# Optimization experiments

Measured on AMD Instinct MI355X. Metric: run time of the kernel, lower is better.

Reference implementation:

```python
import jax, jax.numpy as jnp
import numpy as np

N = 50000      # nodes
E = 800000     # edges
IN = 128       # raw node feature dim
EMB = 64       # gene/pathway embedding dim
H = 256        # hidden dim
R = 12         # relations
B = 8          # num_bases (hardcoded in HRAN)
HEADS = 4      # attention heads (hardcoded)
NG = 20000     # n_gene
NPATH = 2000   # n_path
IN1 = IN + EMB # conv1 input dim


def _glorot(k, shape):
    fan_in, fan_out = shape[-2], shape[-1]
    s = np.sqrt(2.0 / (fan_in + fan_out)).astype(np.float32)
    return jax.random.normal(k, shape, jnp.float32) * s


def setup_inputs() -> dict:
    key = jax.random.key(0)
    ks = jax.random.split(key, 20)
    return {
        "x": jax.random.normal(ks[0], (N, IN), jnp.float32),
        "edge_index": jax.random.randint(ks[1], (2, E), 0, N),
        "edge_type": jax.random.randint(ks[2], (E,), 0, R),
        "gene_idx": jnp.arange(NG),
        "path_idx": jnp.arange(NPATH) + NG,  # disjoint from gene_idx
        "gene_emb": jax.random.normal(ks[3], (NG, EMB), jnp.float32) * 0.02,
        "path_emb": jax.random.normal(ks[4], (NPATH, EMB), jnp.float32) * 0.02,
        "comp1": _glorot(ks[5], (R, B)),
        "basis1": _glorot(ks[6], (B, IN1, H)),
        "root1": _glorot(ks[7], (IN1, H)),
        "bias1": jnp.zeros((H,), jnp.float32),
        "att1": _glorot(ks[8], (HEADS, H // HEADS)),
        "comp2": _glorot(ks[9], (R, B)),
        "basis2": _glorot(ks[10], (B, H, H)),
        "root2": _glorot(ks[11], (H, H)),
        "bias2": jnp.zeros((H,), jnp.float32),
        "att2": _glorot(ks[12], (HEADS, H // HEADS)),
        "pred_w": _glorot(ks[13], (H, 12)),
        "pred_b": jnp.zeros((12,), jnp.float32),
    }


def _rgcn(x, src, dst, et, comp, basis, root, bias):
    # Basis-decomposed RGCN with per-relation mean aggregation (PyG default).
    flat = dst * R + et                                   # combined (node, rel) id
    cnt = jax.ops.segment_sum(jnp.ones((src.shape[0],), jnp.float32), flat,
                              num_segments=N * R)
    w = 1.0 / jnp.maximum(cnt[flat], 1.0)                 # [E] mean normalizer
    coeff = comp[et] * w[:, None]                         # [E, B]
    xs = x[src]                                           # [E, in]  gather
    # aggregate in input space, then one dense contraction with the bases
    agg = jnp.stack([jax.ops.segment_sum(coeff[:, b, None] * xs, dst,
                                         num_segments=N)
                     for b in range(B)], axis=1)          # [N, B, in]
    return jnp.einsum('nbi,bio->no', agg, basis) + x @ root + bias


def _hran_conv(x, src, dst, et, comp, basis, root, bias, att):
    h = _rgcn(x, src, dst, et, comp, basis, root, bias)
    h = h.reshape(N, HEADS, -1)                           # [N, heads, hd]
    alpha = jax.nn.softmax((h * att).sum(-1), axis=1)     # softmax over heads
    return (h * alpha[..., None]).reshape(N, -1)


def reference(x, edge_index, edge_type, gene_idx, path_idx,
              gene_emb, path_emb,
              comp1, basis1, root1, bias1, att1,
              comp2, basis2, root2, bias2, att2,
              pred_w, pred_b):
    src, dst = edge_index[0], edge_index[1]
    x0 = jnp.concatenate([x, jnp.zeros((N, EMB), x.dtype)], axis=1)
    x0 = x0.at[gene_idx, IN:].add(gene_emb)
    x0 = x0.at[path_idx, IN:].add(path_emb)
    h = _hran_conv(x0, src, dst, edge_type, comp1, basis1, root1, bias1, att1)
    h = _hran_conv(h, src, dst, edge_type, comp2, basis2, root2, bias2, att2)
    return h @ pred_w + pred_b                            # [N, 12]
```

## Files before the change

kernel.cpp:

```cpp
#include <hip/hip_runtime.h>
#include <cstddef>

#define NN     50000
#define NE     800000
#define IND    128
#define EMBD   64
#define IN1    192
#define HDIM   256
#define RR     12
#define BB     8
#define NGENE  20000
#define NPATH  2000
#define NRK    (RR * NN)
#define SCB    1024
#define NSB    ((NRK + SCB - 1) / SCB)
#define CHA    16704
#define CHB    33408
#define CH2N   (NN - CHB)

typedef __attribute__((ext_vector_type(8))) short short8;
typedef __attribute__((ext_vector_type(4))) float f32x4;
typedef unsigned short ushortT;
typedef __attribute__((address_space(3))) void lds_void;
typedef __attribute__((address_space(1))) const void glb_void;

__device__ __forceinline__ float bu2f(unsigned short u) {
  unsigned int x = ((unsigned int)u) << 16;
  return __builtin_bit_cast(float, x);
}
__device__ __forceinline__ unsigned short f2bu(float f) {
  unsigned int x = __builtin_bit_cast(unsigned int, f);
  unsigned int r = (x + 0x7fffu + ((x >> 16) & 1u)) >> 16;
  return (unsigned short)r;
}


__global__ void k_build_x0(const float* __restrict__ x, ushortT* __restrict__ x0) {
  int t = blockIdx.x * 256 + threadIdx.x;
  if (t >= NN * IN1) return;
  int n = t / IN1, i = t - n * IN1;
  float v = (i < IND) ? x[(size_t)n * IND + i] : 0.0f;
  int kt = i >> 6, ch = (i >> 3) & 7, off = i & 7;
  x0[(size_t)n * IN1 + kt * 64 + ((ch ^ (n & 7)) * 8) + off] = f2bu(v);
}

__global__ void k_add_emb(const int* __restrict__ idx, const float* __restrict__ emb,
                          ushortT* __restrict__ x0, int count) {
  int t = blockIdx.x * 256 + threadIdx.x;
  if (t >= count * EMBD) return;
  int g = t / EMBD, j = t - g * EMBD;
  int n = idx[g];
  int ch = (j >> 3) & 7, off = j & 7;
  x0[(size_t)n * IN1 + 128 + ((ch ^ (n & 7)) * 8) + off] = f2bu(emb[t]);
}

__global__ void k_count(const int* __restrict__ ei, const int* __restrict__ et,
                        int* __restrict__ cnt) {
  int e = blockIdx.x * 256 + threadIdx.x;
  if (e >= NE) return;
  atomicAdd(&cnt[ei[NE + e] * RR + et[e]], 1);
}

__global__ __launch_bounds__(256) void k_scan1(const int* __restrict__ cnt,
                                               int* __restrict__ bsum) {
  __shared__ int lds[256];
  int t = threadIdx.x;
  int base = blockIdx.x * SCB + t * 4;
  int s = 0;
#pragma unroll
  for (int j = 0; j < 4; j++) { int idx = base + j; if (idx < NRK) s += cnt[idx]; }
  lds[t] = s; __syncthreads();
  for (int d = 128; d > 0; d >>= 1) { if (t < d) lds[t] += lds[t + d]; __syncthreads(); }
  if (t == 0) bsum[blockIdx.x] = lds[0];
}

__global__ __launch_bounds__(1024) void k_scan2(const int* __restrict__ bsum,
                                                int* __restrict__ bscan) {
  __shared__ int lds[1024];
  int t = threadIdx.x;
  int v = (t < NSB) ? bsum[t] : 0;
  lds[t] = v; __syncthreads();
  for (int d = 1; d < 1024; d <<= 1) {
    int add = (t >= d) ? lds[t - d] : 0; __syncthreads();
    lds[t] += add; __syncthreads();
  }
  if (t < NSB) bscan[t] = lds[t] - v;
}

__global__ __launch_bounds__(256) void k_scan3(const int* __restrict__ cnt,
                                               const int* __restrict__ bscan,
                                               int* __restrict__ off) {
  __shared__ int lds[256];
  int t = threadIdx.x;
  int base = blockIdx.x * SCB + t * 4;
  int v[4]; int s = 0;
#pragma unroll
  for (int j = 0; j < 4; j++) { int idx = base + j; v[j] = (idx < NRK) ? cnt[idx] : 0; s += v[j]; }
  lds[t] = s; __syncthreads();
  for (int d = 1; d < 256; d <<= 1) {
    int add = (t >= d) ? lds[t - d] : 0; __syncthreads();
    lds[t] += add; __syncthreads();
  }
  int ex = lds[t] - s + bscan[blockIdx.x];
#pragma unroll
  for (int j = 0; j < 4; j++) {
    int idx = base + j;
    if (idx < NRK) { off[idx] = ex; ex += v[j]; }
  }
}

__global__ void k_fill(const int* __restrict__ ei, const int* __restrict__ et,
                       const int* __restrict__ off, int* __restrict__ fill,
                       int* __restrict__ srcs) {
  int e = blockIdx.x * 256 + threadIdx.x;
  if (e >= NE) return;
  int key = ei[NE + e] * RR + et[e];
  int pos = off[key] + atomicAdd(&fill[key], 1);
  srcs[pos] = ei[e];
}

__global__ void k_wbasis(const float* __restrict__ basis, ushortT* __restrict__ W,
                         int in_dim) {
  int t = blockIdx.x * 256 + threadIdx.x;
  int total = BB * HDIM * in_dim;
  if (t >= total) return;
  int i = t % in_dim;
  int o = (t / in_dim) & 255;
  int b = t / (in_dim * 256);
  W[t] = f2bu(basis[((size_t)b * in_dim + i) * HDIM + o]);
}

__global__ void k_troot(const float* __restrict__ root, ushortT* __restrict__ rt,
                        int in_dim) {
  int t = blockIdx.x * 256 + threadIdx.x;
  if (t >= in_dim * HDIM) return;
  int i = t % in_dim, o = t / in_dim;
  rt[t] = f2bu(root[(size_t)i * HDIM + o]);
}


__device__ __forceinline__ void dev_aggb(const int* __restrict__ srcs,
                                         const int* __restrict__ off,
                                         const int* __restrict__ cnt,
                                         const float* __restrict__ comp,
                                         const ushortT* __restrict__ xin,
                                         ushortT* __restrict__ aggB,
                                         int in_dim, int row0, int nrows,
                                         int li, int lane) {
  if (li >= nrows) return;
  int dst = row0 + li;
  bool act = lane * 4 < in_dim;
  int kt = lane >> 4, chl = (lane >> 1) & 7, offh = (lane & 1) * 4;
  int kbase = kt * 64 + offh;

  auto gaddr = [&](int s) {
    return (const ushort4*)(xin + (size_t)s * in_dim + kbase + ((chl ^ (s & 7)) * 8));
  };

  int beg[RR], n[RR];
#pragma unroll
  for (int rl = 0; rl < RR; rl++) {
    beg[rl] = off[dst * RR + rl];
    n[rl]   = cnt[dst * RR + rl];
  }

  int sa[RR], sb[RR];
#pragma unroll
  for (int rl = 0; rl < RR; rl++) {
    sa[rl] = (n[rl] > 0) ? srcs[beg[rl]] : 0;
    sb[rl] = (n[rl] > 1) ? srcs[beg[rl] + 1] : 0;
  }

  ushort4 va[RR], vb[RR];
  if (act) {
#pragma unroll
    for (int rl = 0; rl < RR; rl++) va[rl] = *gaddr(sa[rl]);
#pragma unroll
    for (int rl = 0; rl < RR; rl++) vb[rl] = *gaddr(sb[rl]);
  }

  float acc[BB][4];
#pragma unroll
  for (int b = 0; b < BB; b++)
#pragma unroll
    for (int e = 0; e < 4; e++) acc[b][e] = 0.f;

#pragma unroll
  for (int rl = 0; rl < RR; rl++) {
    int ne = n[rl];
    if (ne == 0) continue;
    float s0 = 0.f, s1 = 0.f, s2 = 0.f, s3 = 0.f;
    if (act) {
      s0 = bu2f(va[rl].x); s1 = bu2f(va[rl].y); s2 = bu2f(va[rl].z); s3 = bu2f(va[rl].w);
      if (ne > 1) {
        s0 += bu2f(vb[rl].x); s1 += bu2f(vb[rl].y);
        s2 += bu2f(vb[rl].z); s3 += bu2f(vb[rl].w);
      }
    }
    for (int p = 2; p < ne; p++) {
      int s = srcs[beg[rl] + p];
      if (act) {
        ushort4 v = *gaddr(s);
        s0 += bu2f(v.x); s1 += bu2f(v.y); s2 += bu2f(v.z); s3 += bu2f(v.w);
      }
    }
    float wn = 1.0f / (float)ne;
#pragma unroll
    for (int b = 0; b < BB; b++) {
      float cb = comp[rl * BB + b] * wn;
      acc[b][0] += cb * s0; acc[b][1] += cb * s1;
      acc[b][2] += cb * s2; acc[b][3] += cb * s3;
    }
  }

  if (act) {
    size_t base = (size_t)li * BB * in_dim;
    int swz = (chl ^ (dst & 7)) * 8;
#pragma unroll
    for (int b = 0; b < BB; b++) {
      ushort4 o;
      o.x = f2bu(acc[b][0]); o.y = f2bu(acc[b][1]);
      o.z = f2bu(acc[b][2]); o.w = f2bu(acc[b][3]);
      *(ushort4*)(aggB + base + (size_t)b * in_dim + kbase + swz) = o;
    }
  }
}

__device__ __forceinline__ void dev_gemm(ushortT* As , float (*sm)[4],
                                         int gblk, int tid,
                                         const ushortT* __restrict__ xin,
                                         const ushortT* __restrict__ aggB,
                                         const ushortT* __restrict__ W,
                                         const float* __restrict__ bias,
                                         const float* __restrict__ att,
                                         ushortT* __restrict__ hout,
                                         int in_dim, int row0, int row1) {
  const int bm = row0 + gblk * 64;
  const int wv = tid >> 6, l = tid & 63;
  const int wc = wv;
  const int lm = l & 15, lq = l >> 4;
  const int nkt = in_dim >> 6;
  const int totKt = 9 * nkt;

  f32x4 acc[4][4];
#pragma unroll
  for (int mt = 0; mt < 4; mt++)
#pragma unroll
    for (int nt = 0; nt < 4; nt++) acc[mt][nt] = (f32x4){0.f, 0.f, 0.f, 0.f};

  struct WF { short8 f[2][4]; };
  WF w0, w1;

  auto stage = [&](int buf, int seg, int kt) {
#pragma unroll
    for (int j = 0; j < 2; j++) {
      int r = wv * 16 + j * 8;
      int g = bm + r + (l >> 3); if (g >= row1) g = row1 - 1;
      const ushortT* gp;
      if (seg == 0) gp = xin + (size_t)g * in_dim + kt * 64 + (l & 7) * 8;
      else gp = aggB + ((size_t)(g - row0) * 8 + (seg - 1)) * in_dim + kt * 64 + (l & 7) * 8;
      ushortT* lp = &As[(size_t)buf * 64 * 64 + r * 64];
      __builtin_amdgcn_global_load_lds((glb_void*)gp, (lds_void*)lp, 16, 0, 0);
    }
  };

  auto loadW = [&](WF& wd, int seg, int kt) {
    const ushortT* wt = W + (size_t)(wc * 64 + lm) * in_dim +
                        (size_t)seg * 256 * in_dim + kt * 64 + lq * 8;
#pragma unroll
    for (int nt = 0; nt < 4; nt++) {
      wd.f[0][nt] = *(const short8*)(wt + (size_t)nt * 16 * in_dim);
      wd.f[1][nt] = *(const short8*)(wt + (size_t)nt * 16 * in_dim + 32);
    }
  };

  auto mfmaT = [&](int buf, const WF& wf) {
#pragma unroll
    for (int ks = 0; ks < 2; ks++) {
      short8 af[4];
#pragma unroll
      for (int mt = 0; mt < 4; mt++) {
        int ar = mt * 16 + lm;
        af[mt] = *(const short8*)(&As[(size_t)buf * 64 * 64 + ar * 64 +
                                      (((ks * 4) + lq) ^ (ar & 7)) * 8]);
      }
#pragma unroll
      for (int mt = 0; mt < 4; mt++)
#pragma unroll
        for (int nt = 0; nt < 4; nt++)
          acc[mt][nt] = __builtin_amdgcn_mfma_f32_16x16x32_bf16(af[mt], wf.f[ks][nt],
                                                                acc[mt][nt], 0, 0, 0);
    }
  };

  int segS = 0, ktS = 0;
  int segW = 0, ktW = 0;
  auto bumpC = [&](int& s, int& k) {
    if (++k == nkt) { k = 0; if (++s == 9) { s = 8; k = nkt - 1; } }
  };

  auto body = [&](int t, WF& wuse, WF& wload) {
    loadW(wload, segW, ktW); bumpC(segW, ktW);
    asm volatile("s_waitcnt vmcnt(10)" ::: "memory");
    __builtin_amdgcn_s_barrier();
    __builtin_amdgcn_sched_barrier(0);
    stage((t + 3) & 3, segS, ktS); bumpC(segS, ktS);
    mfmaT(t & 3, wuse);
  };

  stage(0, segS, ktS); bumpC(segS, ktS);
  stage(1, segS, ktS); bumpC(segS, ktS);
  stage(2, segS, ktS); bumpC(segS, ktS);
  loadW(w0, segW, ktW); bumpC(segW, ktW);

  int t = 0;
  for (; t + 1 < totKt; t += 2) {
    body(t, w0, w1);
    body(t + 1, w1, w0);
  }
  if (t < totKt) body(t, w0, w1);
  asm volatile("s_waitcnt vmcnt(0)" ::: "memory");
  __syncthreads();

  float bv[4];
#pragma unroll
  for (int nt = 0; nt < 4; nt++) bv[nt] = bias[wc * 64 + nt * 16 + lm];
#pragma unroll
  for (int mt = 0; mt < 4; mt++)
#pragma unroll
    for (int nt = 0; nt < 4; nt++)
#pragma unroll
      for (int r = 0; r < 4; r++) acc[mt][nt][r] += bv[nt];

  float av[4];
#pragma unroll
  for (int nt = 0; nt < 4; nt++) av[nt] = att[wc * 64 + nt * 16 + lm];
#pragma unroll
  for (int mt = 0; mt < 4; mt++) {
    float sr[4];
#pragma unroll
    for (int r = 0; r < 4; r++)
      sr[r] = acc[mt][0][r] * av[0] + acc[mt][1][r] * av[1] +
              acc[mt][2][r] * av[2] + acc[mt][3][r] * av[3];
#pragma unroll
    for (int o = 1; o <= 8; o <<= 1) {
#pragma unroll
      for (int r = 0; r < 4; r++) sr[r] += __shfl_xor(sr[r], o, 64);
    }
    if (lm == 0) {
#pragma unroll
      for (int r = 0; r < 4; r++) sm[mt * 16 + lq * 4 + r][wc] = sr[r];
    }
  }
  __syncthreads();
  if (tid < 64) {
    float s0 = sm[tid][0], s1 = sm[tid][1], s2 = sm[tid][2], s3 = sm[tid][3];
    float mx = fmaxf(fmaxf(s0, s1), fmaxf(s2, s3));
    float e0 = __expf(s0 - mx), e1 = __expf(s1 - mx), e2 = __expf(s2 - mx), e3 = __expf(s3 - mx);
    float inv = 1.0f / (e0 + e1 + e2 + e3);
    sm[tid][0] = e0 * inv; sm[tid][1] = e1 * inv; sm[tid][2] = e2 * inv; sm[tid][3] = e3 * inv;
  }
  __syncthreads();
#pragma unroll
  for (int mt = 0; mt < 4; mt++) {
#pragma unroll
    for (int r = 0; r < 4; r++) {
      int rl = mt * 16 + lq * 4 + r;
      int row = bm + rl;
      if (row >= row1) continue;
      float al = sm[rl][wc];
      ushortT* op = hout + (size_t)row * HDIM + wc * 64;
      int key = row & 7;
#pragma unroll
      for (int nt = 0; nt < 4; nt++) {
        int ci = nt * 16 + lm;
        op[(((ci >> 3) ^ key) * 8) + (ci & 7)] = f2bu(acc[mt][nt][r] * al);
      }
    }
  }
}


__global__ __launch_bounds__(256) void k_aggb(const int* __restrict__ srcs,
                                              const int* __restrict__ off,
                                              const int* __restrict__ cnt,
                                              const float* __restrict__ comp,
                                              const ushortT* __restrict__ xin,
                                              ushortT* __restrict__ aggB,
                                              int in_dim, int row0, int nrows) {
  int wv = threadIdx.x >> 6, lane = threadIdx.x & 63;
  dev_aggb(srcs, off, cnt, comp, xin, aggB, in_dim, row0, nrows,
           blockIdx.x * 4 + wv, lane);
}

__global__ __launch_bounds__(256, 2) void k_gemm(const ushortT* __restrict__ xin,
                                                 const ushortT* __restrict__ aggB,
                                                 const ushortT* __restrict__ W,
                                                 const float* __restrict__ bias,
                                                 const float* __restrict__ att,
                                                 ushortT* __restrict__ hout,
                                                 int in_dim, int row0, int row1) {
  __shared__ ushortT As[4][64 * 64];
  __shared__ float sm[64][4];
  dev_gemm(&As[0][0], sm, blockIdx.x, threadIdx.x,
           xin, aggB, W, bias, att, hout, in_dim, row0, row1);
}

__global__ __launch_bounds__(256, 2) void k_fused(const ushortT* __restrict__ xin,
                                                  const ushortT* __restrict__ aggR,
                                                  const ushortT* __restrict__ W,
                                                  const float* __restrict__ bias,
                                                  const float* __restrict__ att,
                                                  ushortT* __restrict__ hout,
                                                  int in_dim, int grow0, int grow1,
                                                  int gB,
                                                  const int* __restrict__ srcs,
                                                  const int* __restrict__ off,
                                                  const int* __restrict__ cnt,
                                                  const float* __restrict__ comp,
                                                  ushortT* __restrict__ aggW,
                                                  int arow0, int anrows) {
  __shared__ ushortT As[4][64 * 64];
  __shared__ float sm[64][4];
  if ((int)blockIdx.x < gB) {
    dev_gemm(&As[0][0], sm, blockIdx.x, threadIdx.x,
             xin, aggR, W, bias, att, hout, in_dim, grow0, grow1);
  } else {
    int wv = threadIdx.x >> 6, lane = threadIdx.x & 63;
    dev_aggb(srcs, off, cnt, comp, xin, aggW, in_dim, arow0, anrows,
             ((int)blockIdx.x - gB) * 4 + wv, lane);
  }
}

__global__ void k_pred(const ushortT* __restrict__ h, const float* __restrict__ w,
                       const float* __restrict__ b, float* __restrict__ out) {
  int t = blockIdx.x * 256 + threadIdx.x;
  if (t >= NN * 12) return;
  int n = t / 12, j = t - n * 12;
  float acc = b[j];
  const ushortT* hp = h + (size_t)n * HDIM;
  int key = n & 7;
#pragma unroll
  for (int kt = 0; kt < 4; kt++)
#pragma unroll
    for (int cs = 0; cs < 8; cs++) {
      int ch = cs ^ key;
      int kb = kt * 64 + ch * 8;
      const ushortT* hh = hp + kt * 64 + cs * 8;
#pragma unroll
      for (int o = 0; o < 8; o++) acc += bu2f(hh[o]) * w[(kb + o) * 12 + j];
    }
  out[t] = acc;
}

extern "C" void kernel_launch(void* const* d_in, const int* in_sizes, int n_in,
                              void* d_out, int out_size, void* d_ws, size_t ws_size,
                              hipStream_t stream) {
  const float* x         = (const float*)d_in[0];
  const int*   edge_idx  = (const int*)d_in[1];
  const int*   edge_type = (const int*)d_in[2];
  const int*   gene_idx  = (const int*)d_in[3];
  const int*   path_idx  = (const int*)d_in[4];
  const float* gene_emb  = (const float*)d_in[5];
  const float* path_emb  = (const float*)d_in[6];
  const float* comp1     = (const float*)d_in[7];
  const float* basis1    = (const float*)d_in[8];
  const float* root1     = (const float*)d_in[9];
  const float* bias1     = (const float*)d_in[10];
  const float* att1      = (const float*)d_in[11];
  const float* comp2     = (const float*)d_in[12];
  const float* basis2    = (const float*)d_in[13];
  const float* root2     = (const float*)d_in[14];
  const float* bias2     = (const float*)d_in[15];
  const float* att2      = (const float*)d_in[16];
  const float* pred_w    = (const float*)d_in[17];
  const float* pred_b    = (const float*)d_in[18];
  float* out = (float*)d_out;

  char* ws = (char*)d_ws;
  ushortT* x0b   = (ushortT*)(ws);
  ushortT* h2b   = (ushortT*)(ws);
  ushortT* h1b   = (ushortT*)(ws + 25600000);
  ushortT* aggB0 = (ushortT*)(ws + 51200000);
  ushortT* aggB1 = (ushortT*)(ws + 119619584);
  ushortT* Wb1   = (ushortT*)(ws + 188039168);
  ushortT* Wb2   = (ushortT*)(ws + 188923904);
  int*     cnt   = (int*)(ws + 190103552);
  int*     off   = (int*)(ws + 192503552);
  int*     srcs  = (int*)(ws + 194903552);
  int*     fill  = (int*)(ws + 198103552);
  int*     bsum  = (int*)(ws + 200503552);
  int*     bscan = (int*)(ws + 200507648);

  dim3 blk(256);

  k_build_x0<<<dim3((NN * IN1) / 256), blk, 0, stream>>>(x, x0b);
  k_add_emb<<<dim3((NGENE * EMBD) / 256), blk, 0, stream>>>(gene_idx, gene_emb, x0b, NGENE);
  k_add_emb<<<dim3((NPATH * EMBD) / 256), blk, 0, stream>>>(path_idx, path_emb, x0b, NPATH);
  hipMemsetAsync(cnt, 0, NRK * 4, stream);
  hipMemsetAsync(fill, 0, NRK * 4, stream);
  k_count<<<dim3(NE / 256), blk, 0, stream>>>(edge_idx, edge_type, cnt);
  k_scan1<<<dim3(NSB), blk, 0, stream>>>(cnt, bsum);
  k_scan2<<<dim3(1), dim3(1024), 0, stream>>>(bsum, bscan);
  k_scan3<<<dim3(NSB), blk, 0, stream>>>(cnt, bscan, off);
  k_fill<<<dim3(NE / 256), blk, 0, stream>>>(edge_idx, edge_type, off, fill, srcs);
  k_troot<<<dim3((IN1 * HDIM) / 256), blk, 0, stream>>>(root1, Wb1, IN1);
  k_troot<<<dim3((HDIM * HDIM) / 256), blk, 0, stream>>>(root2, Wb2, HDIM);
  k_wbasis<<<dim3((BB * HDIM * IN1) / 256), blk, 0, stream>>>(basis1, Wb1 + 256 * IN1, IN1);
  k_wbasis<<<dim3((BB * HDIM * HDIM) / 256), blk, 0, stream>>>(basis2, Wb2 + 256 * HDIM, HDIM);

  const int gB01 = CHA / 64;
  const int gB2  = (CH2N + 63) / 64;
  const int aB01 = CHA / 4;
  const int aB2  = (CH2N + 3) / 4;

  k_aggb<<<dim3(aB01), blk, 0, stream>>>(srcs, off, cnt, comp1, x0b, aggB0, IN1, 0, CHA);
  k_fused<<<dim3(gB01 + aB01), blk, 0, stream>>>(x0b, aggB0, Wb1, bias1, att1, h1b,
                                                 IN1, 0, CHA, gB01,
                                                 srcs, off, cnt, comp1, aggB1, CHA, CHA);
  k_fused<<<dim3(gB01 + aB2), blk, 0, stream>>>(x0b, aggB1, Wb1, bias1, att1, h1b,
                                                IN1, CHA, CHB, gB01,
                                                srcs, off, cnt, comp1, aggB0, CHB, CH2N);
  k_gemm<<<dim3(gB2), blk, 0, stream>>>(x0b, aggB0, Wb1, bias1, att1, h1b, IN1, CHB, NN);

  k_aggb<<<dim3(aB01), blk, 0, stream>>>(srcs, off, cnt, comp2, h1b, aggB0, HDIM, 0, CHA);
  k_fused<<<dim3(gB01 + aB01), blk, 0, stream>>>(h1b, aggB0, Wb2, bias2, att2, h2b,
                                                 HDIM, 0, CHA, gB01,
                                                 srcs, off, cnt, comp2, aggB1, CHA, CHA);
  k_fused<<<dim3(gB01 + aB2), blk, 0, stream>>>(h1b, aggB1, Wb2, bias2, att2, h2b,
                                                HDIM, CHA, CHB, gB01,
                                                srcs, off, cnt, comp2, aggB0, CHB, CH2N);
  k_gemm<<<dim3(gB2), blk, 0, stream>>>(h1b, aggB0, Wb2, bias2, att2, h2b, HDIM, CHB, NN);

  k_pred<<<dim3((NN * 12 + 255) / 256), blk, 0, stream>>>(h2b, pred_w, pred_b, out);
}
```

Before: 915.4 us.

## Co-schedule aggregation waves inside GEMM blocks and split into two chunks

Replaces the three-chunk pipeline, which used separate GEMM and aggregation blocks, with a two-chunk scheme. In layer 1 each 512-thread block runs the GEMM on waves 0-3 while waves 4-7 aggregate the next chunk, matching the GEMM's barrier count with s_barrier calls. Layer 2 drops the fusion and runs plain sequential aggregate/GEMM pairs. The workspace is re-laid-out for the larger aggregation buffers. The aim is tighter overlap of memory-bound gathers with MFMA work within a CU. The cost is reliance on exact barrier matching and doubled per-block register pressure.

```diff
diff --git a/kernel.cpp b/kernel.cpp
--- a/kernel.cpp
+++ b/kernel.cpp
@@ -14,9 +14,7 @@
 #define NRK    (RR * NN)
 #define SCB    1024
 #define NSB    ((NRK + SCB - 1) / SCB)
-#define CHA    16704
-#define CHB    33408
-#define CH2N   (NN - CHB)
+#define CH0    25088
 
 typedef __attribute__((ext_vector_type(8))) short short8;
 typedef __attribute__((ext_vector_type(4))) float f32x4;
@@ -139,15 +137,14 @@
 }
 
 
-__device__ __forceinline__ void dev_aggb(const int* __restrict__ srcs,
-                                         const int* __restrict__ off,
-                                         const int* __restrict__ cnt,
-                                         const float* __restrict__ comp,
-                                         const ushortT* __restrict__ xin,
-                                         ushortT* __restrict__ aggB,
-                                         int in_dim, int row0, int nrows,
-                                         int li, int lane) {
-  if (li >= nrows) return;
+__device__ __forceinline__ void dev_agg_one(const int* __restrict__ srcs,
+                                            const int* __restrict__ off,
+                                            const int* __restrict__ cnt,
+                                            const float* __restrict__ comp,
+                                            const ushortT* __restrict__ xin,
+                                            ushortT* __restrict__ aggB,
+                                            int in_dim, int row0,
+                                            int li, int lane) {
   int dst = row0 + li;
   bool act = lane * 4 < in_dim;
   int kt = lane >> 4, chl = (lane >> 1) & 7, offh = (lane & 1) * 4;
@@ -389,8 +386,9 @@
                                               ushortT* __restrict__ aggB,
                                               int in_dim, int row0, int nrows) {
   int wv = threadIdx.x >> 6, lane = threadIdx.x & 63;
-  dev_aggb(srcs, off, cnt, comp, xin, aggB, in_dim, row0, nrows,
-           blockIdx.x * 4 + wv, lane);
+  int li = blockIdx.x * 4 + wv;
+  if (li < nrows)
+    dev_agg_one(srcs, off, cnt, comp, xin, aggB, in_dim, row0, li, lane);
 }
 
 __global__ __launch_bounds__(256, 2) void k_gemm(const ushortT* __restrict__ xin,
@@ -406,14 +404,13 @@
            xin, aggB, W, bias, att, hout, in_dim, row0, row1);
 }
 
-__global__ __launch_bounds__(256, 2) void k_fused(const ushortT* __restrict__ xin,
+__global__ __launch_bounds__(512, 2) void k_gfuse(const ushortT* __restrict__ xin,
                                                   const ushortT* __restrict__ aggR,
                                                   const ushortT* __restrict__ W,
                                                   const float* __restrict__ bias,
                                                   const float* __restrict__ att,
                                                   ushortT* __restrict__ hout,
                                                   int in_dim, int grow0, int grow1,
-                                                  int gB,
                                                   const int* __restrict__ srcs,
                                                   const int* __restrict__ off,
                                                   const int* __restrict__ cnt,
@@ -422,13 +419,25 @@
                                                   int arow0, int anrows) {
   __shared__ ushortT As[4][64 * 64];
   __shared__ float sm[64][4];
-  if ((int)blockIdx.x < gB) {
-    dev_gemm(&As[0][0], sm, blockIdx.x, threadIdx.x,
+  const int tid = threadIdx.x;
+  if (tid < 256) {
+    dev_gemm(&As[0][0], sm, blockIdx.x, tid,
              xin, aggR, W, bias, att, hout, in_dim, grow0, grow1);
   } else {
-    int wv = threadIdx.x >> 6, lane = threadIdx.x & 63;
-    dev_aggb(srcs, off, cnt, comp, xin, aggW, in_dim, arow0, anrows,
-             ((int)blockIdx.x - gB) * 4 + wv, lane);
+    const int totKt = 9 * (in_dim >> 6);
+    const int wv4 = (tid >> 6) - 4;
+    const int lane = tid & 63;
+    for (int i = 0; i < totKt; i++) {
+      __builtin_amdgcn_s_barrier();
+      if (i < 16) {
+        int li = blockIdx.x * 64 + i * 4 + wv4;
+        if (li < anrows)
+          dev_agg_one(srcs, off, cnt, comp, xin, aggW, in_dim, arow0, li, lane);
+      }
+    }
+    __builtin_amdgcn_s_barrier();
+    __builtin_amdgcn_s_barrier();
+    __builtin_amdgcn_s_barrier();
   }
 }
 
@@ -482,15 +491,15 @@
   ushortT* h2b   = (ushortT*)(ws);
   ushortT* h1b   = (ushortT*)(ws + 25600000);
   ushortT* aggB0 = (ushortT*)(ws + 51200000);
-  ushortT* aggB1 = (ushortT*)(ws + 119619584);
-  ushortT* Wb1   = (ushortT*)(ws + 188039168);
-  ushortT* Wb2   = (ushortT*)(ws + 188923904);
-  int*     cnt   = (int*)(ws + 190103552);
-  int*     off   = (int*)(ws + 192503552);
-  int*     srcs  = (int*)(ws + 194903552);
-  int*     fill  = (int*)(ws + 198103552);
-  int*     bsum  = (int*)(ws + 200503552);
-  int*     bscan = (int*)(ws + 200507648);
+  ushortT* aggB1 = (ushortT*)(ws + 153960448);
+  ushortT* Wb1   = (ushortT*)(ws + 230490112);
+  ushortT* Wb2   = (ushortT*)(ws + 231374848);
+  int*     cnt   = (int*)(ws + 232554496);
+  int*     off   = (int*)(ws + 234954496);
+  int*     srcs  = (int*)(ws + 237354496);
+  int*     fill  = (int*)(ws + 51200000);
+  int*     bsum  = (int*)(ws + 53600000);
+  int*     bscan = (int*)(ws + 53604096);
 
   dim3 blk(256);
 
@@ -509,28 +518,21 @@
   k_wbasis<<<dim3((BB * HDIM * IN1) / 256), blk, 0, stream>>>(basis1, Wb1 + 256 * IN1, IN1);
   k_wbasis<<<dim3((BB * HDIM * HDIM) / 256), blk, 0, stream>>>(basis2, Wb2 + 256 * HDIM, HDIM);
 
-  const int gB01 = CHA / 64;
-  const int gB2  = (CH2N + 63) / 64;
-  const int aB01 = CHA / 4;
-  const int aB2  = (CH2N + 3) / 4;
-
-  k_aggb<<<dim3(aB01), blk, 0, stream>>>(srcs, off, cnt, comp1, x0b, aggB0, IN1, 0, CHA);
-  k_fused<<<dim3(gB01 + aB01), blk, 0, stream>>>(x0b, aggB0, Wb1, bias1, att1, h1b,
-                                                 IN1, 0, CHA, gB01,
-                                                 srcs, off, cnt, comp1, aggB1, CHA, CHA);
-  k_fused<<<dim3(gB01 + aB2), blk, 0, stream>>>(x0b, aggB1, Wb1, bias1, att1, h1b,
-                                                IN1, CHA, CHB, gB01,
-                                                srcs, off, cnt, comp1, aggB0, CHB, CH2N);
-  k_gemm<<<dim3(gB2), blk, 0, stream>>>(x0b, aggB0, Wb1, bias1, att1, h1b, IN1, CHB, NN);
-
-  k_aggb<<<dim3(aB01), blk, 0, stream>>>(srcs, off, cnt, comp2, h1b, aggB0, HDIM, 0, CHA);
-  k_fused<<<dim3(gB01 + aB01), blk, 0, stream>>>(h1b, aggB0, Wb2, bias2, att2, h2b,
-                                                 HDIM, 0, CHA, gB01,
-                                                 srcs, off, cnt, comp2, aggB1, CHA, CHA);
-  k_fused<<<dim3(gB01 + aB2), blk, 0, stream>>>(h1b, aggB1, Wb2, bias2, att2, h2b,
-                                                HDIM, CHA, CHB, gB01,
-                                                srcs, off, cnt, comp2, aggB0, CHB, CH2N);
-  k_gemm<<<dim3(gB2), blk, 0, stream>>>(h1b, aggB0, Wb2, bias2, att2, h2b, HDIM, CHB, NN);
+  const int n1 = CH0;
+  const int n2 = NN - CH0;
+  const int g1 = n1 / 64;
+  const int g2 = (n2 + 63) / 64;
+
+  k_aggb<<<dim3(n1 / 4), blk, 0, stream>>>(srcs, off, cnt, comp1, x0b, aggB0, IN1, 0, n1);
+  k_gfuse<<<dim3(g1), dim3(512), 0, stream>>>(x0b, aggB0, Wb1, bias1, att1, h1b,
+                                              IN1, 0, CH0,
+                                              srcs, off, cnt, comp1, aggB1, CH0, n2);
+  k_gemm<<<dim3(g2), blk, 0, stream>>>(x0b, aggB1, Wb1, bias1, att1, h1b, IN1, CH0, NN);
+
+  k_aggb<<<dim3(n1 / 4), blk, 0, stream>>>(srcs, off, cnt, comp2, h1b, aggB0, HDIM, 0, n1);
+  k_gemm<<<dim3(g1), blk, 0, stream>>>(h1b, aggB0, Wb2, bias2, att2, h2b, HDIM, 0, CH0);
+  k_aggb<<<dim3((n2 + 3) / 4), blk, 0, stream>>>(srcs, off, cnt, comp2, h1b, aggB0, HDIM, CH0, n2);
+  k_gemm<<<dim3(g2), blk, 0, stream>>>(h1b, aggB0, Wb2, bias2, att2, h2b, HDIM, CH0, NN);
 
   k_pred<<<dim3((NN * 12 + 255) / 256), blk, 0, stream>>>(h2b, pred_w, pred_b, out);
 }
```

After: 925.7 us. Within noise of the previous version (+1.1%).
